# Optimization experiments

Measured on AMD Instinct MI355X. Metric: run time of the kernel, lower is better.

Reference implementation:

```python
import jax, jax.numpy as jnp
import numpy as np

KS = 7
HEADS = 8


def _conv1x1(a, w, b):
    # a: (B,Cin,H,W), w: (Cout,Cin), b: (Cout,)
    return jnp.einsum('bchw,oc->bohw', a, w) + b[None, :, None, None]


def _unfold2d(a, ks):
    # a: (B,C,Hp,Wp) -> (B,C,H,W,ks,ks) sliding windows, stride 1
    H = a.shape[2] - ks + 1
    W = a.shape[3] - ks + 1
    ii = jnp.arange(H)[:, None] + jnp.arange(ks)[None, :]  # (H,ks)
    jj = jnp.arange(W)[:, None] + jnp.arange(ks)[None, :]  # (W,ks)
    return a[:, :, ii[:, None, :, None], jj[None, :, None, :]]


def setup_inputs() -> dict:
    key = jax.random.key(0)
    ks = jax.random.split(key, 10)
    B, C, H, W = 4, 128, 56, 56
    x = jax.random.normal(ks[0], (B, C, H, W), dtype=jnp.float32)
    sc = 1.0 / np.sqrt(C)
    q_w = jax.random.normal(ks[1], (C, C), dtype=jnp.float32) * sc
    q_b = jax.random.normal(ks[2], (C,), dtype=jnp.float32) * 0.01
    k_w = jax.random.normal(ks[3], (C, C), dtype=jnp.float32) * sc
    k_b = jax.random.normal(ks[4], (C,), dtype=jnp.float32) * 0.01
    v_w = jax.random.normal(ks[5], (C, C), dtype=jnp.float32) * sc
    v_b = jax.random.normal(ks[6], (C,), dtype=jnp.float32) * 0.01
    rel_h = jax.random.normal(ks[7], (C // 2, KS, 1), dtype=jnp.float32)
    rel_w = jax.random.normal(ks[8], (C // 2, 1, KS), dtype=jnp.float32)
    return {'x': x, 'q_w': q_w, 'q_b': q_b, 'k_w': k_w, 'k_b': k_b,
            'v_w': v_w, 'v_b': v_b, 'rel_h': rel_h, 'rel_w': rel_w}


def reference(x, q_w, q_b, k_w, k_b, v_w, v_b, rel_h, rel_w):
    B, C, H, W = x.shape
    dkh = C // HEADS
    K2 = KS * KS
    pl = (KS - 1) // 2
    pr = KS - 1 - pl
    xp = jnp.pad(x, ((0, 0), (0, 0), (pl, pr), (pl, pr)))

    k = _conv1x1(xp, k_w, k_b)
    v = _conv1x1(xp, v_w, v_b)
    q = _conv1x1(x, q_w, q_b)

    # unfold K/V into (B,C,H,W,KS,KS) then reshape exactly as torch does
    # (this reshape intermixes channel/window axes; replicated faithfully)
    k6 = _unfold2d(k, KS).reshape(B, HEADS, H, W, dkh, K2)
    v6 = _unfold2d(v, KS).reshape(B, HEADS, H, W, dkh, K2)
    q6 = q.reshape(B, HEADS, H, W, dkh, 1)

    # q^T k over the dkh axis -> (B,heads,H,W,KS,KS)
    qk = jnp.einsum('bhxyd,bhxydk->bhxyk', q6[..., 0], k6)
    qk = qk.reshape(B, HEADS, H, W, KS, KS)

    # einsum 'bhxydz,cij->bhxyij' has no shared index: factorizes as
    # (sum over d,z of q) * (sum over c of rel)
    qsum = q6.sum(axis=(4, 5))  # (B,heads,H,W)
    qk = qk + qsum[..., None, None] * rel_h.sum(axis=0)  # (KS,1) broadcast
    qk = qk + qsum[..., None, None] * rel_w.sum(axis=0)  # (1,KS) broadcast

    w = jax.nn.softmax(qk.reshape(B, HEADS, H, W, K2), axis=-1)
    out = jnp.einsum('bhxyk,bhxydk->bhxyd', w, v6)  # (B,heads,H,W,dvh)
    return out.reshape(B, C, H, W)
```

## Files before the change

kernel.cpp:

```cpp
#include <hip/hip_runtime.h>
#include <hip/hip_bf16.h>
#include <math.h>

#define NB    4
#define NC    128
#define NPIX  3136
#define CHW   401408
#define SKS   68
#define STS   19

template <int CTRL, int RM>
__device__ __forceinline__ float dpp_mov(float x, float old) {
    return __int_as_float(__builtin_amdgcn_update_dpp(
        __float_as_int(old), __float_as_int(x), CTRL, RM, 0xf, false));
}
__device__ __forceinline__ float wave_max(float x) {
    x = fmaxf(x, dpp_mov<0x111, 0xf>(x, x));
    x = fmaxf(x, dpp_mov<0x112, 0xf>(x, x));
    x = fmaxf(x, dpp_mov<0x114, 0xf>(x, x));
    x = fmaxf(x, dpp_mov<0x118, 0xf>(x, x));
    x = fmaxf(x, dpp_mov<0x142, 0xa>(x, x));
    x = fmaxf(x, dpp_mov<0x143, 0xc>(x, x));
    return __int_as_float(__builtin_amdgcn_readlane(__float_as_int(x), 63));
}
__device__ __forceinline__ float wave_sum(float x) {
    x = x + dpp_mov<0x111, 0xf>(x, 0.f);
    x = x + dpp_mov<0x112, 0xf>(x, 0.f);
    x = x + dpp_mov<0x114, 0xf>(x, 0.f);
    x = x + dpp_mov<0x118, 0xf>(x, 0.f);
    x = x + dpp_mov<0x142, 0xa>(x, 0.f);
    x = x + dpp_mov<0x143, 0xc>(x, 0.f);
    return __int_as_float(__builtin_amdgcn_readlane(__float_as_int(x), 63));
}

__global__ __launch_bounds__(256) void prep_kernel(
    const float* __restrict__ qw, const float* __restrict__ kw,
    const float* __restrict__ vw,
    const float* __restrict__ rel_h, const float* __restrict__ rel_w,
    float* __restrict__ w4q, float* __restrict__ w4k, float* __restrict__ w4v,
    float* __restrict__ rb)
{
    int idx = blockIdx.x * 256 + threadIdx.x;
    if (idx < 3 * 16384) {
        int m = idx >> 14;
        int r = idx & 16383;
        int cc = r & 3;
        int t = r >> 2;
        int o = t & 127;
        int c4 = t >> 7;
        const float* src = (m == 0) ? qw : (m == 1) ? kw : vw;
        float* dst = (m == 0) ? w4q : (m == 1) ? w4k : w4v;
        dst[r] = src[o * 128 + c4 * 4 + cc];
    }
    if (idx < 14) {
        const float* src = (idx < 7) ? rel_h : rel_w;
        int off = (idx < 7) ? idx : idx - 7;
        float s = 0.f;
        for (int c = 0; c < 64; ++c) s += src[c * 7 + off];
        rb[idx] = s;
    }
}

__global__ __launch_bounds__(256) void conv_kernel(
    const float* __restrict__ x,
    const float* __restrict__ w4q, const float* __restrict__ w4k,
    const float* __restrict__ w4v,
    const float* __restrict__ qb, const float* __restrict__ kb,
    const float* __restrict__ vb,
    float* __restrict__ q, float* __restrict__ kbuf, float* __restrict__ vbuf)
{
    __shared__ float sx[128 * 16];
    __shared__ float st[3 * 128 * STS];
    int bid = blockIdx.x;
    int tile = bid % 196;
    int b = bid / 196;
    int pix0 = tile * 16;
    const float* xb = x + b * CHW + pix0;

    for (int i = threadIdx.x; i < 512; i += 256) {
        int c = i >> 2, p4 = (i & 3) * 4;
        *(float4*)(sx + c * 16 + p4) = *(const float4*)(xb + c * NPIX + p4);
    }
    __syncthreads();

    int lane = threadIdx.x & 63;
    int wave = threadIdx.x >> 6;
    int o = wave * 32 + (lane & 31);
    int ph = (lane >> 5) * 8;
    const float4* Wq = (const float4*)w4q + o;
    const float4* Wk = (const float4*)w4k + o;
    const float4* Wv = (const float4*)w4v + o;

    float4 wqc = Wq[0], wkc = Wk[0], wvc = Wv[0];
    float aq[8] = {}, ak[8] = {}, av[8] = {};
    #pragma unroll 1
    for (int c4 = 0; c4 < 32; ++c4) {
        float4 xs[8];
        #pragma unroll
        for (int cc = 0; cc < 4; ++cc) {
            xs[2 * cc]     = *(const float4*)(sx + (c4 * 4 + cc) * 16 + ph);
            xs[2 * cc + 1] = *(const float4*)(sx + (c4 * 4 + cc) * 16 + ph + 4);
        }
        float4 wq4 = wqc, wk4 = wkc, wv4 = wvc;
        if (c4 < 31) {
            wqc = Wq[(c4 + 1) * 128];
            wkc = Wk[(c4 + 1) * 128];
            wvc = Wv[(c4 + 1) * 128];
        }
        float wqr[4] = {wq4.x, wq4.y, wq4.z, wq4.w};
        float wkr[4] = {wk4.x, wk4.y, wk4.z, wk4.w};
        float wvr[4] = {wv4.x, wv4.y, wv4.z, wv4.w};
        #pragma unroll
        for (int cc = 0; cc < 4; ++cc) {
            float4 xa = xs[2 * cc], xc = xs[2 * cc + 1];
            float xv[8] = {xa.x, xa.y, xa.z, xa.w, xc.x, xc.y, xc.z, xc.w};
            #pragma unroll
            for (int p = 0; p < 8; ++p) {
                aq[p] += wqr[cc] * xv[p];
                ak[p] += wkr[cc] * xv[p];
                av[p] += wvr[cc] * xv[p];
            }
        }
    }
    float bq = qb[o], bk = kb[o], bv = vb[o];
    float* wrq = st + o * STS + ph;
    float* wrk = st + 128 * STS + o * STS + ph;
    float* wrv = st + 2 * 128 * STS + o * STS + ph;
    #pragma unroll
    for (int p = 0; p < 8; ++p) {
        wrq[p] = aq[p] + bq;
        wrk[p] = ak[p] + bk;
        wrv[p] = av[p] + bv;
    }
    __syncthreads();

    int pix = threadIdx.x & 15;
    int o8 = (threadIdx.x >> 4) * 8;
    float* qd = q + b * CHW + pix0 + pix;
    float* kd = kbuf + b * CHW + pix0 + pix;
    float* vd = vbuf + b * CHW + pix0 + pix;
    #pragma unroll
    for (int i = 0; i < 8; ++i) {
        int r = o8 + i;
        qd[r * NPIX] = st[r * STS + pix];
        kd[r * NPIX] = st[128 * STS + r * STS + pix];
        vd[r * NPIX] = st[2 * 128 * STS + r * STS + pix];
    }
}

__global__ __launch_bounds__(256) void attn_kernel(
    const float* __restrict__ q, const float* __restrict__ kbuf,
    const float* __restrict__ vbuf,
    const float* __restrict__ kb, const float* __restrict__ vb,
    const float* __restrict__ rb, float* __restrict__ out)
{
    __shared__ float sK[20 * SKS];
    __shared__ float sV[21 * SKS];
    __shared__ float sW[4 * 64];
    int bid = blockIdx.x;
    int qpart = bid & 3;
    int bc = bid >> 2;
    int ch = bc & 127;
    const float* qc = q + bc * NPIX + 784 * qpart;
    const float* kc = kbuf + bc * NPIX;
    const float* vc = vbuf + bc * NPIX;
    float* oc = out + bc * NPIX + 784 * qpart;
    float kbias = kb[ch], vbias = vb[ch];
    int qr0 = 14 * qpart;

    for (int i = threadIdx.x; i < 20 * 62; i += 256) {
        int yy = i / 62, xx = i - yy * 62;
        int gy = qr0 + yy - 3;
        int gx = xx - 3;
        bool in = (gy >= 0) && (gy < 56) && (gx >= 0) && (gx < 56);
        int off = in ? gy * 56 + gx : 0;
        float kv = in ? kc[off] : kbias;
        float vv = in ? vc[off] : vbias;
        sK[yy * SKS + xx] = kv;
        sV[yy * SKS + xx] = vv;
    }
    for (int i = threadIdx.x; i < SKS; i += 256) sV[20 * SKS + i] = 0.f;
    __syncthreads();

    int lane = threadIdx.x & 63;
    int wave = threadIdx.x >> 6;
    int k2 = min(lane, 48);
    int di = k2 / 7, dj = k2 - di * 7;
    float rbias = rb[di] + rb[7 + dj];
    int koff = di * SKS + dj;
    int t16 = lane & 15, p = lane >> 4;
    float* sWw = sW + wave * 64;

    int ulu = __builtin_amdgcn_readfirstlane(wave * 16);
    float4 p0 = *(const float4*)(qc + ulu);
    float4 p1 = *(const float4*)(qc + ulu + 4);
    float4 p2 = *(const float4*)(qc + ulu + 8);
    float4 p3 = *(const float4*)(qc + ulu + 12);

    for (int gl = wave; gl < 49; gl += 4) {
        int ul0 = gl * 16;
        int y0 = ul0 / 56;
        int x0 = ul0 - y0 * 56;

        float4 q0 = p0, q1 = p1, q2 = p2, q3 = p3;
        if (gl + 4 < 49) {
            int un = __builtin_amdgcn_readfirstlane((gl + 4) * 16);
            p0 = *(const float4*)(qc + un);
            p1 = *(const float4*)(qc + un + 4);
            p2 = *(const float4*)(qc + un + 8);
            p3 = *(const float4*)(qc + un + 12);
        }
        float qa[16] = {q0.x, q0.y, q0.z, q0.w, q1.x, q1.y, q1.z, q1.w,
                        q2.x, q2.y, q2.z, q2.w, q3.x, q3.y, q3.z, q3.w};
        float qs = 0.f;
        #pragma unroll
        for (int t = 0; t < 16; ++t) qs += qa[t];

        float acc = 0.f;
        const float* kb_ = sK + y0 * SKS + x0 + koff;
        if (x0 != 48) {
            #pragma unroll
            for (int t = 0; t < 16; ++t) acc += qa[t] * kb_[t];
        } else {
            const float* kb2 = sK + (y0 + 1) * SKS + koff;
            #pragma unroll
            for (int t = 0; t < 8; ++t) acc += qa[t] * kb_[t];
            #pragma unroll
            for (int t = 0; t < 8; ++t) acc += qa[8 + t] * kb2[t];
        }
        float val = (lane < 49) ? (acc + qs * rbias) : -1e30f;

        float mS = wave_max(val);
        float e = __expf(val - mS);
        float sS = wave_sum(e);
        float wgt = e * __builtin_amdgcn_rcpf(sS);
        sWw[lane] = wgt;

        int u = ul0 + t16;
        int yt = u / 56;
        int xt = u - yt * 56;
        const float* vbase = sV + yt * SKS + xt + p * (2 * SKS);
        const float* wbase = sWw + p * 14;
        float oacc = 0.f;
        #pragma unroll
        for (int j = 0; j < 7; ++j) oacc += wbase[j] * vbase[j];
        #pragma unroll
        for (int j = 0; j < 7; ++j) oacc += wbase[7 + j] * vbase[SKS + j];
        oacc += __shfl_xor(oacc, 16);
        oacc += __shfl_xor(oacc, 32);
        if (lane < 16) oc[ul0 + lane] = oacc;
    }
}

extern "C" void kernel_launch(void* const* d_in, const int* in_sizes, int n_in,
                              void* d_out, int out_size, void* d_ws, size_t ws_size,
                              hipStream_t stream) {
    const float* x     = (const float*)d_in[0];
    const float* qw    = (const float*)d_in[1];
    const float* qb    = (const float*)d_in[2];
    const float* kw    = (const float*)d_in[3];
    const float* kb    = (const float*)d_in[4];
    const float* vw    = (const float*)d_in[5];
    const float* vb    = (const float*)d_in[6];
    const float* rel_h = (const float*)d_in[7];
    const float* rel_w = (const float*)d_in[8];
    float* out = (float*)d_out;

    float* ws   = (float*)d_ws;
    float* kbuf = ws;
    float* vbuf = kbuf + 1605632;
    float* qbuf = vbuf + 1605632;
    float* w4q  = qbuf + 1605632;
    float* w4k  = w4q + 16384;
    float* w4v  = w4k + 16384;
    float* rb   = w4v + 16384;

    prep_kernel<<<192, 256, 0, stream>>>(qw, kw, vw, rel_h, rel_w,
                                         w4q, w4k, w4v, rb);
    conv_kernel<<<784, 256, 0, stream>>>(x, w4q, w4k, w4v, qb, kb, vb,
                                         qbuf, kbuf, vbuf);
    attn_kernel<<<2048, 256, 0, stream>>>(qbuf, kbuf, vbuf, kb, vb, rb, out);
}
```

Baseline: 72.24 us.

## Store K/V in pre-padded layout so attention loads halo rows with vector loads

```diff
diff --git a/kernel.cpp b/kernel.cpp
--- a/kernel.cpp
+++ b/kernel.cpp
@@ -6,6 +6,7 @@
 #define NC    128
 #define NPIX  3136
 #define CHW   401408
+#define KVP   3968
 #define SKS   68
 #define STS   19
 
@@ -36,11 +37,34 @@
 __global__ __launch_bounds__(256) void prep_kernel(
     const float* __restrict__ qw, const float* __restrict__ kw,
     const float* __restrict__ vw,
+    const float* __restrict__ kb, const float* __restrict__ vb,
     const float* __restrict__ rel_h, const float* __restrict__ rel_w,
+    float* __restrict__ kpad, float* __restrict__ vpad,
     float* __restrict__ w4q, float* __restrict__ w4k, float* __restrict__ w4v,
     float* __restrict__ rb)
 {
     int idx = blockIdx.x * 256 + threadIdx.x;
+    {
+        int img = idx / 708;
+        int hl = idx - img * 708;
+        int p;
+        if (hl < 186) {
+            int r = hl / 62;
+            p = r * 64 + (hl - r * 62);
+        } else if (hl < 372) {
+            int j = hl - 186;
+            int r = j / 62;
+            p = (59 + r) * 64 + (j - r * 62);
+        } else {
+            int j = hl - 372;
+            int r = j / 6, cc = j - r * 6;
+            p = (r + 3) * 64 + (cc < 3 ? cc : cc + 56);
+        }
+        int ch = img & 127;
+        size_t o = (size_t)img * KVP + p;
+        kpad[o] = kb[ch];
+        vpad[o] = vb[ch];
+    }
     if (idx < 3 * 16384) {
         int m = idx >> 14;
         int r = idx & 16383;
@@ -67,7 +91,7 @@
     const float* __restrict__ w4v,
     const float* __restrict__ qb, const float* __restrict__ kb,
     const float* __restrict__ vb,
-    float* __restrict__ q, float* __restrict__ kbuf, float* __restrict__ vbuf)
+    float* __restrict__ q, float* __restrict__ kpad, float* __restrict__ vpad)
 {
     __shared__ float sx[128 * 16];
     __shared__ float st[3 * 128 * STS];
@@ -136,51 +160,53 @@
 
     int pix = threadIdx.x & 15;
     int o8 = (threadIdx.x >> 4) * 8;
+    int pp = pix0 + pix;
+    int yy = pp / 56, xx = pp - yy * 56;
+    int po = (yy + 3) * 64 + xx + 3;
     float* qd = q + b * CHW + pix0 + pix;
-    float* kd = kbuf + b * CHW + pix0 + pix;
-    float* vd = vbuf + b * CHW + pix0 + pix;
+    float* kd = kpad + (size_t)b * 128 * KVP + po;
+    float* vd = vpad + (size_t)b * 128 * KVP + po;
     #pragma unroll
     for (int i = 0; i < 8; ++i) {
         int r = o8 + i;
         qd[r * NPIX] = st[r * STS + pix];
-        kd[r * NPIX] = st[128 * STS + r * STS + pix];
-        vd[r * NPIX] = st[2 * 128 * STS + r * STS + pix];
+        kd[(size_t)r * KVP] = st[128 * STS + r * STS + pix];
+        vd[(size_t)r * KVP] = st[2 * 128 * STS + r * STS + pix];
     }
 }
 
 __global__ __launch_bounds__(256) void attn_kernel(
-    const float* __restrict__ q, const float* __restrict__ kbuf,
-    const float* __restrict__ vbuf,
-    const float* __restrict__ kb, const float* __restrict__ vb,
+    const float* __restrict__ q, const float* __restrict__ kpad,
+    const float* __restrict__ vpad,
     const float* __restrict__ rb, float* __restrict__ out)
 {
-    __shared__ float sK[20 * SKS];
-    __shared__ float sV[21 * SKS];
+    __shared__ __align__(16) float sK[20 * SKS];
+    __shared__ __align__(16) float sV[21 * SKS];
     __shared__ float sW[4 * 64];
     int bid = blockIdx.x;
     int qpart = bid & 3;
     int bc = bid >> 2;
-    int ch = bc & 127;
     const float* qc = q + bc * NPIX + 784 * qpart;
-    const float* kc = kbuf + bc * NPIX;
-    const float* vc = vbuf + bc * NPIX;
     float* oc = out + bc * NPIX + 784 * qpart;
-    float kbias = kb[ch], vbias = vb[ch];
     int qr0 = 14 * qpart;
-
-    for (int i = threadIdx.x; i < 20 * 62; i += 256) {
-        int yy = i / 62, xx = i - yy * 62;
-        int gy = qr0 + yy - 3;
-        int gx = xx - 3;
-        bool in = (gy >= 0) && (gy < 56) && (gx >= 0) && (gx < 56);
-        int off = in ? gy * 56 + gx : 0;
-        float kv = in ? kc[off] : kbias;
-        float vv = in ? vc[off] : vbias;
-        sK[yy * SKS + xx] = kv;
-        sV[yy * SKS + xx] = vv;
+    const float* kp0 = kpad + (size_t)bc * KVP + qr0 * 64;
+    const float* vp0 = vpad + (size_t)bc * KVP + qr0 * 64;
+
+    for (int i = threadIdx.x; i < 320; i += 256) {
+        int yy = i >> 4, c16 = i & 15;
+        if (c16 < 15) {
+            float4 kv4 = *(const float4*)(kp0 + yy * 64 + c16 * 4);
+            float4 vv4 = *(const float4*)(vp0 + yy * 64 + c16 * 4);
+            *(float4*)(sK + yy * SKS + c16 * 4) = kv4;
+            *(float4*)(sV + yy * SKS + c16 * 4) = vv4;
+        } else {
+            float2 kv2 = *(const float2*)(kp0 + yy * 64 + 60);
+            float2 vv2 = *(const float2*)(vp0 + yy * 64 + 60);
+            *(float2*)(sK + yy * SKS + 60) = kv2;
+            *(float2*)(sV + yy * SKS + 60) = vv2;
+        }
     }
     for (int i = threadIdx.x; i < SKS; i += 256) sV[20 * SKS + i] = 0.f;
-    __syncthreads();
 
     int lane = threadIdx.x & 63;
     int wave = threadIdx.x >> 6;
@@ -191,20 +217,18 @@
     int t16 = lane & 15, p = lane >> 4;
     float* sWw = sW + wave * 64;
 
-    int ulu = __builtin_amdgcn_readfirstlane(wave * 16);
-    float4 p0 = *(const float4*)(qc + ulu);
-    float4 p1 = *(const float4*)(qc + ulu + 4);
-    float4 p2 = *(const float4*)(qc + ulu + 8);
-    float4 p3 = *(const float4*)(qc + ulu + 12);
+    int ul0 = wave * 16;
+    int y0 = 0, x0 = ul0;
+    float4 p0 = *(const float4*)(qc + ul0);
+    float4 p1 = *(const float4*)(qc + ul0 + 4);
+    float4 p2 = *(const float4*)(qc + ul0 + 8);
+    float4 p3 = *(const float4*)(qc + ul0 + 12);
+    __syncthreads();
 
     for (int gl = wave; gl < 49; gl += 4) {
-        int ul0 = gl * 16;
-        int y0 = ul0 / 56;
-        int x0 = ul0 - y0 * 56;
-
         float4 q0 = p0, q1 = p1, q2 = p2, q3 = p3;
         if (gl + 4 < 49) {
-            int un = __builtin_amdgcn_readfirstlane((gl + 4) * 16);
+            int un = ul0 + 64;
             p0 = *(const float4*)(qc + un);
             p1 = *(const float4*)(qc + un + 4);
             p2 = *(const float4*)(qc + un + 8);
@@ -241,14 +265,19 @@
         int xt = u - yt * 56;
         const float* vbase = sV + yt * SKS + xt + p * (2 * SKS);
         const float* wbase = sWw + p * 14;
-        float oacc = 0.f;
-        #pragma unroll
-        for (int j = 0; j < 7; ++j) oacc += wbase[j] * vbase[j];
-        #pragma unroll
-        for (int j = 0; j < 7; ++j) oacc += wbase[7 + j] * vbase[SKS + j];
+        float o0 = 0.f, o1 = 0.f;
+        #pragma unroll
+        for (int j = 0; j < 7; ++j) o0 += wbase[j] * vbase[j];
+        #pragma unroll
+        for (int j = 0; j < 7; ++j) o1 += wbase[7 + j] * vbase[SKS + j];
+        float oacc = o0 + o1;
         oacc += __shfl_xor(oacc, 16);
         oacc += __shfl_xor(oacc, 32);
         if (lane < 16) oc[ul0 + lane] = oacc;
+
+        ul0 += 64;
+        x0 += 8; y0 += 1;
+        if (x0 >= 56) { x0 -= 56; ++y0; }
     }
 }
 
@@ -267,17 +296,17 @@
     float* out = (float*)d_out;
 
     float* ws   = (float*)d_ws;
-    float* kbuf = ws;
-    float* vbuf = kbuf + 1605632;
-    float* qbuf = vbuf + 1605632;
+    float* kpad = ws;
+    float* vpad = kpad + 2031616;
+    float* qbuf = vpad + 2031616;
     float* w4q  = qbuf + 1605632;
     float* w4k  = w4q + 16384;
     float* w4v  = w4k + 16384;
     float* rb   = w4v + 16384;
 
-    prep_kernel<<<192, 256, 0, stream>>>(qw, kw, vw, rel_h, rel_w,
-                                         w4q, w4k, w4v, rb);
+    prep_kernel<<<1416, 256, 0, stream>>>(qw, kw, vw, kb, vb, rel_h, rel_w,
+                                          kpad, vpad, w4q, w4k, w4v, rb);
     conv_kernel<<<784, 256, 0, stream>>>(x, w4q, w4k, w4v, qb, kb, vb,
-                                         qbuf, kbuf, vbuf);
-    attn_kernel<<<2048, 256, 0, stream>>>(qbuf, kbuf, vbuf, kb, vb, rb, out);
-}
+                                         qbuf, kpad, vpad);
+    attn_kernel<<<2048, 256, 0, stream>>>(qbuf, kpad, vpad, rb, out);
+}
```

Measured after the change: 76.37 us. +5.7%, slower.
